# Kernel tuning notes

Measured on AMD Instinct MI355X. Metric: run time of the kernel, lower is better.

The kernel has to match this reference:

```python
import jax, jax.numpy as jnp
import numpy as np

# Attention(d_model=1024, d_head=64, h=16, fastmax=True) -> fastmax_custom path with
# mask=True, normalize=True, temperature=1, a0=1, a1=1, lim=1, p=1, zero RPE.
B, N, D_MODEL, H, D_HEAD = 1, 2048, 1024, 16, 64
A0, A1, LIM = 1.0, 1.0, 1.0


def setup_inputs() -> dict:
    key = jax.random.key(0)
    ks = jax.random.split(key, 6)
    s = 1.0 / np.sqrt(D_MODEL).astype(np.float32)
    return {
        "X": jax.random.normal(ks[0], (B, N, D_MODEL), jnp.float32),
        "Wq": jax.random.normal(ks[1], (H * D_HEAD, D_MODEL), jnp.float32) * s,
        "Wk": jax.random.normal(ks[2], (H * D_HEAD, D_MODEL), jnp.float32) * s,
        "Wv": jax.random.normal(ks[3], (H * D_HEAD, D_MODEL), jnp.float32) * s,
        "Wo": jax.random.normal(ks[4], (D_MODEL, H * D_HEAD), jnp.float32) * s,
        "bo": jnp.zeros((D_MODEL,), jnp.float32),
    }


def _fastmax_causal_p1(q, k, v):
    # q,k,v: [b,h,n,d]. fastmax normalize: scale q,k so the max per-token L2 norm
    # (over the sequence, per batch-head) equals LIM; temperature forced to 1.
    qn = jnp.max(jnp.linalg.norm(q, axis=-1), axis=-1)[..., None, None]  # [b,h,1,1]
    kn = jnp.max(jnp.linalg.norm(k, axis=-1), axis=-1)[..., None, None]
    q = LIM * q / qn
    k = LIM * k / kn
    n = q.shape[2]
    # first-order (p=1) polynomial kernel attention, causal via prefix sums:
    #   score(i,j) = a0 + a1 * <q_i, k_j>,  j <= i
    kv = jnp.cumsum(k[..., :, None] * v[..., None, :], axis=2)  # [b,h,n,d,d]
    num = A0 * jnp.cumsum(v, axis=2) + A1 * jnp.einsum('bhnd,bhnde->bhne', q, kv)
    ksum = jnp.cumsum(k, axis=2)  # [b,h,n,d]
    den = A0 * jnp.arange(1, n + 1, dtype=q.dtype) + A1 * jnp.einsum('bhnd,bhnd->bhn', q, ksum)
    return num / den[..., None]


def reference(X, Wq, Wk, Wv, Wo, bo):
    b, n, _ = X.shape

    def heads(W):
        # [b,n,d_model] @ [d_model,h*d] -> [b,h,n,d]
        return (X @ W.T).reshape(b, n, H, D_HEAD).transpose(0, 2, 1, 3)

    q, k, v = heads(Wq), heads(Wk), heads(Wv)
    vh = _fastmax_causal_p1(q, k, v)                       # [b,h,n,d]
    vh = vh.transpose(0, 2, 1, 3).reshape(b, n, H * D_HEAD)
    return vh @ Wo.T + bo                                  # eval mode: dropout is identity
```

## Files before the change

### kernel.cpp

```cpp
#include <hip/hip_runtime.h>

#define N_SEQ 2048
#define NH 16
#define DH 64
#define CHUNK 64
#define NCHUNK 32

typedef float f32x4 __attribute__((ext_vector_type(4)));
typedef __bf16 bf16x8 __attribute__((ext_vector_type(8)));
typedef unsigned short u16x4 __attribute__((ext_vector_type(4)));
typedef unsigned short u16x8 __attribute__((ext_vector_type(8)));

static __device__ inline unsigned short f2b(float x) {
    unsigned int u = __builtin_bit_cast(unsigned int, x);
    unsigned int r = (u + 0x7fffu + ((u >> 16) & 1u)) >> 16;
    return (unsigned short)r;
}
static __device__ inline float b2f(unsigned short b) {
    return __builtin_bit_cast(float, (unsigned int)b << 16);
}
static __device__ inline int sw(int row, int col) {
    return row * 64 + (col ^ ((row & 7) << 3));
}

__global__ __launch_bounds__(256) void cast_all(
    const float* __restrict__ X, const float* __restrict__ Wq, const float* __restrict__ Wk,
    const float* __restrict__ Wv, const float* __restrict__ Wo,
    unsigned short* __restrict__ Xb, unsigned short* __restrict__ Wb,
    unsigned short* __restrict__ Wob, float* __restrict__ nrm) {
    if (blockIdx.x == 0 && threadIdx.x < 32) nrm[threadIdx.x] = 0.f;
    int i = blockIdx.x * 256 + threadIdx.x;
    const float* src; unsigned short* dst; int off;
    if (i < 524288)       { src = X;  dst = Xb;               off = i; }
    else if (i < 786432)  { src = Wq; dst = Wb;               off = i - 524288; }
    else if (i < 1048576) { src = Wk; dst = Wb + (1u << 20);  off = i - 786432; }
    else if (i < 1310720) { src = Wv; dst = Wb + (2u << 20);  off = i - 1048576; }
    else                  { src = Wo; dst = Wob;              off = i - 1310720; }
    float4 v = reinterpret_cast<const float4*>(src)[off];
    u16x4 o;
    o[0] = f2b(v.x); o[1] = f2b(v.y); o[2] = f2b(v.z); o[3] = f2b(v.w);
    reinterpret_cast<u16x4*>(dst)[off] = o;
}

static __device__ inline void gload_lds16(const unsigned short* g, unsigned short* l) {
    __builtin_amdgcn_global_load_lds(
        (const __attribute__((address_space(1))) unsigned int*)g,
        (__attribute__((address_space(3))) unsigned int*)l, 16, 0, 0);
}

template<int MODE, int BM>
__global__ __launch_bounds__(256, 2) void gemm_bf16(
    const unsigned short* __restrict__ A,
    const unsigned short* __restrict__ B,
    float* __restrict__ outf,
    unsigned short* __restrict__ outb,
    const float* __restrict__ bias,
    float* __restrict__ nrm,
    int M, int N, int K)
{
    __shared__ __align__(16) unsigned short As[BM][64];
    __shared__ __align__(16) unsigned short Bs[128][64];

    const int L = blockIdx.y * gridDim.x + blockIdx.x;
    const int cpx = (gridDim.x * gridDim.y) >> 3;
    const int tile = (L & 7) * cpx + (L >> 3);
    const int bn = tile / gridDim.y;
    const int bm = tile % gridDim.y;

    const int t = threadIdx.x;
    const int wave = t >> 6, lane = t & 63;
    const int wm = wave >> 1, wn = wave & 1;
    const int r16 = lane & 15, ks = lane >> 4;
    constexpr int MFRAG = BM / 32;

    f32x4 acc[MFRAG][4] = {};

    const unsigned short* gA = A + (size_t)bm * BM * K;
    const unsigned short* gB = B + (size_t)bn * 128 * K;
    const int lrow = lane >> 3;
    const int scol = (((lane & 7) ^ (lrow & 7)) << 3);
    const int rsw = (r16 & 7) << 3;

    for (int k0 = 0; k0 < K; k0 += 64) {
        __syncthreads();
        #pragma unroll
        for (int g = 0; g < BM / 32; ++g) {
            int r0 = wave * (BM / 4) + g * 8;
            gload_lds16(&gA[(size_t)(r0 + lrow) * K + k0 + scol], &As[r0][0]);
        }
        #pragma unroll
        for (int g = 0; g < 4; ++g) {
            int r0 = wave * 32 + g * 8;
            gload_lds16(&gB[(size_t)(r0 + lrow) * K + k0 + scol], &Bs[r0][0]);
        }
        __syncthreads();

        #pragma unroll
        for (int ksub = 0; ksub < 2; ++ksub) {
            const int sl = (((ksub << 2) + ks) << 3) ^ rsw;
            bf16x8 af[MFRAG], bfr[4];
            #pragma unroll
            for (int m = 0; m < MFRAG; ++m)
                af[m] = *reinterpret_cast<const bf16x8*>(&As[wm * (BM / 2) + m * 16 + r16][sl]);
            #pragma unroll
            for (int n = 0; n < 4; ++n)
                bfr[n] = *reinterpret_cast<const bf16x8*>(&Bs[wn * 64 + n * 16 + r16][sl]);
            #pragma unroll
            for (int m = 0; m < MFRAG; ++m)
                #pragma unroll
                for (int n = 0; n < 4; ++n)
                    acc[m][n] = __builtin_amdgcn_mfma_f32_16x16x32_bf16(af[m], bfr[n], acc[m][n], 0, 0, 0);
        }
    }

    #pragma unroll
    for (int m = 0; m < MFRAG; ++m) {
        int row0 = bm * BM + wm * (BM / 2) + m * 16 + ks * 4;
        #pragma unroll
        for (int n = 0; n < 4; ++n) {
            int col = bn * 128 + wn * 64 + n * 16 + r16;
            if (MODE == 0) {
                int wch = col >> 10, h = (col >> 6) & 15, d = col & 63;
                unsigned short* dst = outb + (size_t)wch * (NH * (size_t)N_SEQ * DH)
                                          + (size_t)h * N_SEQ * DH + d;
                #pragma unroll
                for (int j = 0; j < 4; ++j)
                    dst[(size_t)(row0 + j) * DH] = f2b(acc[m][n][j]);
            } else {
                float bv = bias[col];
                #pragma unroll
                for (int j = 0; j < 4; ++j)
                    outf[(size_t)(row0 + j) * N + col] = acc[m][n][j] + bv;
            }
        }
    }

    if (MODE == 0) {
        const int colbase = bn * 128 + wn * 64;
        const int wch = colbase >> 10;
        if (wch < 2) {
            const int h = (colbase >> 6) & 15;
            float mx = 0.f;
            #pragma unroll
            for (int m = 0; m < MFRAG; ++m)
                #pragma unroll
                for (int j = 0; j < 4; ++j) {
                    float rs = 0.f;
                    #pragma unroll
                    for (int n = 0; n < 4; ++n) rs = fmaf(acc[m][n][j], acc[m][n][j], rs);
                    rs += __shfl_xor(rs, 1);
                    rs += __shfl_xor(rs, 2);
                    rs += __shfl_xor(rs, 4);
                    rs += __shfl_xor(rs, 8);
                    mx = fmaxf(mx, rs);
                }
            mx = fmaxf(mx, __shfl_xor(mx, 16));
            mx = fmaxf(mx, __shfl_xor(mx, 32));
            if (lane == 0)
                atomicMax(reinterpret_cast<unsigned int*>(&nrm[wch * 16 + h]),
                          __builtin_bit_cast(unsigned int, mx));
        }
    }
}

__global__ __launch_bounds__(256) void chunk_sums(const unsigned short* __restrict__ Kb,
                                                  const unsigned short* __restrict__ Vb,
                                                  unsigned short* __restrict__ Ssum,
                                                  float* __restrict__ zsum,
                                                  float* __restrict__ vssum) {
    const int h = blockIdx.x >> 5, c = blockIdx.x & 31;
    __shared__ __align__(16) unsigned short Kt[4096];
    __shared__ __align__(16) unsigned short Vt[4096];
    const size_t off = ((size_t)h * N_SEQ + c * CHUNK) * DH;
    const int t = threadIdx.x, lane = t & 63;

    {
        const int d = t & 63, j0 = (t >> 6) * 16;
        unsigned short rk[16], rv[16];
        #pragma unroll
        for (int i = 0; i < 16; ++i) {
            rk[i] = Kb[off + (size_t)(j0 + i) * DH + d];
            rv[i] = Vb[off + (size_t)(j0 + i) * DH + d];
        }
        u16x8 a, b;
        #pragma unroll
        for (int i = 0; i < 8; ++i) { a[i] = rk[i]; b[i] = rk[8 + i]; }
        *reinterpret_cast<u16x8*>(&Kt[sw(d, j0)]) = a;
        *reinterpret_cast<u16x8*>(&Kt[sw(d, j0 + 8)]) = b;
        #pragma unroll
        for (int i = 0; i < 8; ++i) { a[i] = rv[i]; b[i] = rv[8 + i]; }
        *reinterpret_cast<u16x8*>(&Vt[sw(d, j0)]) = a;
        *reinterpret_cast<u16x8*>(&Vt[sw(d, j0 + 8)]) = b;
    }
    __syncthreads();

    const int w = t >> 6, cl = lane & 15, g = lane >> 4;
    bf16x8 ak0 = *reinterpret_cast<const bf16x8*>(&Kt[sw(w * 16 + cl, g * 8)]);
    bf16x8 ak1 = *reinterpret_cast<const bf16x8*>(&Kt[sw(w * 16 + cl, 32 + g * 8)]);
    f32x4 acc[4] = {};
    #pragma unroll
    for (int et = 0; et < 4; ++et) {
        bf16x8 b0 = *reinterpret_cast<const bf16x8*>(&Vt[sw(et * 16 + cl, g * 8)]);
        bf16x8 b1 = *reinterpret_cast<const bf16x8*>(&Vt[sw(et * 16 + cl, 32 + g * 8)]);
        acc[et] = __builtin_amdgcn_mfma_f32_16x16x32_bf16(ak0, b0, acc[et], 0, 0, 0);
        acc[et] = __builtin_amdgcn_mfma_f32_16x16x32_bf16(ak1, b1, acc[et], 0, 0, 0);
    }
    unsigned short* So = Ssum + (size_t)blockIdx.x * (DH * DH);
    #pragma unroll
    for (int et = 0; et < 4; ++et)
        #pragma unroll
        for (int j = 0; j < 4; ++j)
            So[(size_t)(w * 16 + g * 4 + j) * DH + et * 16 + cl] = f2b(acc[et][j]);

    if (t < 64) {
        float z = 0.f;
        #pragma unroll
        for (int i = 0; i < 8; ++i) {
            u16x8 v = *reinterpret_cast<const u16x8*>(&Kt[sw(t, i * 8)]);
            #pragma unroll
            for (int k = 0; k < 8; ++k) z += b2f(v[k]);
        }
        zsum[(size_t)blockIdx.x * DH + t] = z;
    } else if (t < 128) {
        int e = t - 64;
        float z = 0.f;
        #pragma unroll
        for (int i = 0; i < 8; ++i) {
            u16x8 v = *reinterpret_cast<const u16x8*>(&Vt[sw(e, i * 8)]);
            #pragma unroll
            for (int k = 0; k < 8; ++k) z += b2f(v[k]);
        }
        vssum[(size_t)blockIdx.x * DH + e] = z;
    }
}

__global__ __launch_bounds__(256) void chunk_scan(unsigned short* __restrict__ Ssum,
                                                  float* __restrict__ zsum,
                                                  float* __restrict__ vssum) {
    const int b = blockIdx.x;
    if (b < 256) {
        const int h = b >> 4;
        const int e = (b & 15) * 256 + threadIdx.x;
        size_t base = (size_t)h * NCHUNK * (DH * DH) + e;
        float run = 0.f;
        for (int c = 0; c < NCHUNK; ++c) {
            size_t idx = base + (size_t)c * (DH * DH);
            float tmp = b2f(Ssum[idx]); Ssum[idx] = f2b(run); run += tmp;
        }
    } else {
        const int g = (b - 256) * 256 + threadIdx.x;
        const int which = g >> 10, h = (g >> 6) & 15, e = g & 63;
        float* arr = which ? vssum : zsum;
        size_t base = (size_t)h * NCHUNK * DH + e;
        float run = 0.f;
        for (int c = 0; c < NCHUNK; ++c) {
            size_t idx = base + (size_t)c * DH;
            float tmp = arr[idx]; arr[idx] = run; run += tmp;
        }
    }
}

__global__ __launch_bounds__(256) void intra_attn(
    const unsigned short* __restrict__ Qb, const unsigned short* __restrict__ Kb,
    const unsigned short* __restrict__ Vb,
    const unsigned short* __restrict__ Ssum, const float* __restrict__ zsum,
    const float* __restrict__ vssum, const float* __restrict__ nrm,
    unsigned short* __restrict__ vhb) {
    const int h = blockIdx.x >> 5, c = blockIdx.x & 31;
    __shared__ __align__(16) unsigned short Ql[4096];
    __shared__ __align__(16) unsigned short Kl[4096];
    __shared__ __align__(16) unsigned short Vt[4096];
    __shared__ __align__(16) unsigned short Sp[4096];
    __shared__ __align__(16) unsigned short Pl[4096];
    __shared__ float zp[DH], vsp[DH];

    const int t = threadIdx.x, lane = t & 63, w = t >> 6;
    const float alpha = 1.f / sqrtf(nrm[h] * nrm[16 + h]);
    const size_t off = ((size_t)h * N_SEQ + c * CHUNK) * DH;

    #pragma unroll
    for (int p = 0; p < 2; ++p) {
        int lin = t + p * 256;
        int row = lin >> 3, col = (lin & 7) * 8;
        u16x8 q = *reinterpret_cast<const u16x8*>(Qb + off + (size_t)row * DH + col);
        u16x8 k = *reinterpret_cast<const u16x8*>(Kb + off + (size_t)row * DH + col);
        *reinterpret_cast<u16x8*>(&Ql[sw(row, col)]) = q;
        *reinterpret_cast<u16x8*>(&Kl[sw(row, col)]) = k;
    }
    {
        const int e = t & 63, j0 = (t >> 6) * 16;
        unsigned short rv[16];
        #pragma unroll
        for (int i = 0; i < 16; ++i) rv[i] = Vb[off + (size_t)(j0 + i) * DH + e];
        u16x8 a, b;
        #pragma unroll
        for (int i = 0; i < 8; ++i) { a[i] = rv[i]; b[i] = rv[8 + i]; }
        *reinterpret_cast<u16x8*>(&Vt[sw(e, j0)]) = a;
        *reinterpret_cast<u16x8*>(&Vt[sw(e, j0 + 8)]) = b;
    }
    {
        const unsigned short* Sg = Ssum + (size_t)blockIdx.x * (DH * DH);
        const int e = t & 63, d0 = (t >> 6) * 16;
        u16x8 a, b;
        #pragma unroll
        for (int i = 0; i < 8; ++i) a[i] = f2b(alpha * b2f(Sg[(size_t)(d0 + i) * DH + e]));
        #pragma unroll
        for (int i = 0; i < 8; ++i) b[i] = f2b(alpha * b2f(Sg[(size_t)(d0 + 8 + i) * DH + e]));
        *reinterpret_cast<u16x8*>(&Sp[sw(e, d0)]) = a;
        *reinterpret_cast<u16x8*>(&Sp[sw(e, d0 + 8)]) = b;
    }
    if (t < 64) zp[t] = alpha * zsum[(size_t)blockIdx.x * DH + t];
    else if (t < 128) vsp[t - 64] = vssum[(size_t)blockIdx.x * DH + (t - 64)];
    __syncthreads();

    const int cl = lane & 15, g = lane >> 4;
    const int qrow = (w << 4) + cl;

    bf16x8 aq0 = *reinterpret_cast<const bf16x8*>(&Ql[sw(qrow, g * 8)]);
    bf16x8 aq1 = *reinterpret_cast<const bf16x8*>(&Ql[sw(qrow, 32 + g * 8)]);

    f32x4 acc[4] = {};
    #pragma unroll
    for (int et = 0; et < 4; ++et) {
        bf16x8 b0 = *reinterpret_cast<const bf16x8*>(&Sp[sw(et * 16 + cl, g * 8)]);
        bf16x8 b1 = *reinterpret_cast<const bf16x8*>(&Sp[sw(et * 16 + cl, 32 + g * 8)]);
        acc[et] = __builtin_amdgcn_mfma_f32_16x16x32_bf16(aq0, b0, acc[et], 0, 0, 0);
        acc[et] = __builtin_amdgcn_mfma_f32_16x16x32_bf16(aq1, b1, acc[et], 0, 0, 0);
    }
    f32x4 sacc[4] = {};
    #pragma unroll
    for (int kt = 0; kt < 4; ++kt) {
        bf16x8 b0 = *reinterpret_cast<const bf16x8*>(&Kl[sw(kt * 16 + cl, g * 8)]);
        bf16x8 b1 = *reinterpret_cast<const bf16x8*>(&Kl[sw(kt * 16 + cl, 32 + g * 8)]);
        sacc[kt] = __builtin_amdgcn_mfma_f32_16x16x32_bf16(aq0, b0, sacc[kt], 0, 0, 0);
        sacc[kt] = __builtin_amdgcn_mfma_f32_16x16x32_bf16(aq1, b1, sacc[kt], 0, 0, 0);
    }
    unsigned short* Pw = &Pl[w * 1024];
    float part[4] = {0.f, 0.f, 0.f, 0.f};
    #pragma unroll
    for (int kt = 0; kt < 4; ++kt) {
        int key = kt * 16 + cl;
        #pragma unroll
        for (int j = 0; j < 4; ++j) {
            int rr = g * 4 + j;
            int q = (w << 4) + rr;
            float s = (key <= q) ? fmaf(alpha, sacc[kt][j], 1.f) : 0.f;
            part[j] += s;
            Pw[rr * 64 + (key ^ ((rr & 7) << 3))] = f2b(s);
        }
    }
    #pragma unroll
    for (int j = 0; j < 4; ++j) {
        int q = (w << 4) + g * 4 + j;
        float qz = 0.f;
        #pragma unroll
        for (int m = 0; m < 4; ++m) {
            int d = cl + m * 16;
            qz = fmaf(b2f(Ql[sw(q, d)]), zp[d], qz);
        }
        part[j] += qz;
    }
    #pragma unroll
    for (int o = 1; o < 16; o <<= 1)
        #pragma unroll
        for (int j = 0; j < 4; ++j) part[j] += __shfl_xor(part[j], o);
    float invden[4];
    #pragma unroll
    for (int j = 0; j < 4; ++j) invden[j] = 1.f / ((float)(c * CHUNK) + part[j]);

    #pragma unroll
    for (int ks = 0; ks < 2; ++ks) {
        bf16x8 ap = *reinterpret_cast<const bf16x8*>(&Pw[cl * 64 + ((ks * 32 + g * 8) ^ ((cl & 7) << 3))]);
        #pragma unroll
        for (int et = 0; et < 4; ++et) {
            bf16x8 bv = *reinterpret_cast<const bf16x8*>(&Vt[sw(et * 16 + cl, ks * 32 + g * 8)]);
            acc[et] = __builtin_amdgcn_mfma_f32_16x16x32_bf16(ap, bv, acc[et], 0, 0, 0);
        }
    }
    #pragma unroll
    for (int et = 0; et < 4; ++et)
        #pragma unroll
        for (int j = 0; j < 4; ++j) {
            int q = (w << 4) + g * 4 + j;
            int e = et * 16 + cl;
            float o = (vsp[e] + acc[et][j]) * invden[j];
            vhb[(size_t)(c * CHUNK + q) * (NH * DH) + h * DH + e] = f2b(o);
        }
}

extern "C" void kernel_launch(void* const* d_in, const int* in_sizes, int n_in,
                              void* d_out, int out_size, void* d_ws, size_t ws_size,
                              hipStream_t stream) {
    const float* X  = (const float*)d_in[0];
    const float* Wq = (const float*)d_in[1];
    const float* Wk = (const float*)d_in[2];
    const float* Wv = (const float*)d_in[3];
    const float* Wo = (const float*)d_in[4];
    const float* bo = (const float*)d_in[5];
    float* out = (float*)d_out;

    char* w = (char*)d_ws;
    unsigned short* Xb   = (unsigned short*)(w);
    unsigned short* Wb   = (unsigned short*)(w + (4u  << 20));
    unsigned short* Wob  = (unsigned short*)(w + (10u << 20));
    unsigned short* Qb   = (unsigned short*)(w + (12u << 20));
    unsigned short* vhb  = (unsigned short*)(w + (24u << 20));
    float*          nrm  = (float*)(w + (28u << 20));
    unsigned short* Ssum = (unsigned short*)(w + (29u << 20));
    float*          zsum = (float*)(w + (34u << 20));
    float*          vssum= (float*)(w + (34u << 20) + (1u << 17));
    unsigned short* Kb = Qb + 2097152;
    unsigned short* Vb = Qb + 2u * 2097152;

    cast_all<<<6144, 256, 0, stream>>>(X, Wq, Wk, Wv, Wo, Xb, Wb, Wob, nrm);
    gemm_bf16<0, 128><<<dim3(24, 16), 256, 0, stream>>>(Xb, Wb, nullptr, Qb, nullptr, nrm, 2048, 3072, 1024);
    chunk_sums<<<512, 256, 0, stream>>>(Kb, Vb, Ssum, zsum, vssum);
    chunk_scan<<<264, 256, 0, stream>>>(Ssum, zsum, vssum);
    intra_attn<<<512, 256, 0, stream>>>(Qb, Kb, Vb, Ssum, zsum, vssum, nrm, vhb);
    gemm_bf16<1, 64><<<dim3(8, 32), 256, 0, stream>>>(vhb, Wob, out, nullptr, bo, nullptr, 2048, 1024, 1024);
}
```

Baseline: 68.50 us.

## Double-buffer GEMM LDS tiles and fuse chunk-sum, scan, attention into cooperative kernel

The GEMM now uses two LDS stages and issues the next K-tile's async global-to-LDS loads before computing the current tile, so load latency overlaps MFMA work. The three mid kernels (chunk sums, prefix scan, intra-chunk attention) are merged into one cooperative kernel separated by grid-wide syncs, which removes two launches and reuses the V tile already in LDS. This requires all 512 blocks to be co-resident (2 per CU). Grid syncs add their own overhead, and the doubled LDS in the GEMM may reduce occupancy.

```diff
diff --git a/kernel.cpp b/kernel.cpp
--- a/kernel.cpp
+++ b/kernel.cpp
@@ -1,4 +1,7 @@
 #include <hip/hip_runtime.h>
+#include <hip/hip_cooperative_groups.h>
+
+namespace cg = cooperative_groups;
 
 #define N_SEQ 2048
 #define NH 16
@@ -58,8 +61,8 @@
     float* __restrict__ nrm,
     int M, int N, int K)
 {
-    __shared__ __align__(16) unsigned short As[BM][64];
-    __shared__ __align__(16) unsigned short Bs[128][64];
+    __shared__ __align__(16) unsigned short As[2][BM][64];
+    __shared__ __align__(16) unsigned short Bs[2][128][64];
 
     const int L = blockIdx.y * gridDim.x + blockIdx.x;
     const int cpx = (gridDim.x * gridDim.y) >> 3;
@@ -80,37 +83,45 @@
     const int lrow = lane >> 3;
     const int scol = (((lane & 7) ^ (lrow & 7)) << 3);
     const int rsw = (r16 & 7) << 3;
-
-    for (int k0 = 0; k0 < K; k0 += 64) {
-        __syncthreads();
-        #pragma unroll
-        for (int g = 0; g < BM / 32; ++g) {
-            int r0 = wave * (BM / 4) + g * 8;
-            gload_lds16(&gA[(size_t)(r0 + lrow) * K + k0 + scol], &As[r0][0]);
-        }
-        #pragma unroll
-        for (int g = 0; g < 4; ++g) {
-            int r0 = wave * 32 + g * 8;
-            gload_lds16(&gB[(size_t)(r0 + lrow) * K + k0 + scol], &Bs[r0][0]);
-        }
-        __syncthreads();
-
+    const int NIT = K >> 6;
+
+    auto stage = [&](int it, int pp) {
+        const int k0 = it << 6;
+        #pragma unroll
+        for (int g2 = 0; g2 < BM / 32; ++g2) {
+            int r0 = wave * (BM / 4) + g2 * 8;
+            gload_lds16(&gA[(size_t)(r0 + lrow) * K + k0 + scol], &As[pp][r0][0]);
+        }
+        #pragma unroll
+        for (int g2 = 0; g2 < 4; ++g2) {
+            int r0 = wave * 32 + g2 * 8;
+            gload_lds16(&gB[(size_t)(r0 + lrow) * K + k0 + scol], &Bs[pp][r0][0]);
+        }
+    };
+
+    stage(0, 0);
+    __syncthreads();
+    int pp = 0;
+    for (int it = 0; it < NIT; ++it) {
+        if (it + 1 < NIT) stage(it + 1, pp ^ 1);
         #pragma unroll
         for (int ksub = 0; ksub < 2; ++ksub) {
             const int sl = (((ksub << 2) + ks) << 3) ^ rsw;
             bf16x8 af[MFRAG], bfr[4];
             #pragma unroll
             for (int m = 0; m < MFRAG; ++m)
-                af[m] = *reinterpret_cast<const bf16x8*>(&As[wm * (BM / 2) + m * 16 + r16][sl]);
+                af[m] = *reinterpret_cast<const bf16x8*>(&As[pp][wm * (BM / 2) + m * 16 + r16][sl]);
             #pragma unroll
             for (int n = 0; n < 4; ++n)
-                bfr[n] = *reinterpret_cast<const bf16x8*>(&Bs[wn * 64 + n * 16 + r16][sl]);
+                bfr[n] = *reinterpret_cast<const bf16x8*>(&Bs[pp][wn * 64 + n * 16 + r16][sl]);
             #pragma unroll
             for (int m = 0; m < MFRAG; ++m)
                 #pragma unroll
                 for (int n = 0; n < 4; ++n)
                     acc[m][n] = __builtin_amdgcn_mfma_f32_16x16x32_bf16(af[m], bfr[n], acc[m][n], 0, 0, 0);
         }
+        pp ^= 1;
+        if (it + 1 < NIT) __syncthreads();
     }
 
     #pragma unroll
@@ -163,16 +174,25 @@
     }
 }
 
-__global__ __launch_bounds__(256) void chunk_sums(const unsigned short* __restrict__ Kb,
-                                                  const unsigned short* __restrict__ Vb,
-                                                  unsigned short* __restrict__ Ssum,
-                                                  float* __restrict__ zsum,
-                                                  float* __restrict__ vssum) {
-    const int h = blockIdx.x >> 5, c = blockIdx.x & 31;
-    __shared__ __align__(16) unsigned short Kt[4096];
-    __shared__ __align__(16) unsigned short Vt[4096];
+__global__ __launch_bounds__(256, 2) void mid_kernel(
+    const unsigned short* __restrict__ Qb, const unsigned short* __restrict__ Kb,
+    const unsigned short* __restrict__ Vb,
+    unsigned short* __restrict__ Ssum, float* __restrict__ zsum, float* __restrict__ vssum,
+    const float* __restrict__ nrm, unsigned short* __restrict__ vhb)
+{
+    __shared__ __align__(16) unsigned short sm[5 * 4096];
+    __shared__ float zpvs[2 * DH];
+    unsigned short* s0 = sm;
+    unsigned short* s1 = sm + 4096;
+    unsigned short* s2 = sm + 2 * 4096;
+    unsigned short* s3 = sm + 3 * 4096;
+    unsigned short* s4 = sm + 4 * 4096;
+
+    const int b = blockIdx.x;
+    const int h = b >> 5, c = b & 31;
+    const int t = threadIdx.x, lane = t & 63, w = t >> 6;
     const size_t off = ((size_t)h * N_SEQ + c * CHUNK) * DH;
-    const int t = threadIdx.x, lane = t & 63;
+    const int cl = lane & 15, g = lane >> 4;
 
     {
         const int d = t & 63, j0 = (t >> 6) * 16;
@@ -182,160 +202,126 @@
             rk[i] = Kb[off + (size_t)(j0 + i) * DH + d];
             rv[i] = Vb[off + (size_t)(j0 + i) * DH + d];
         }
-        u16x8 a, b;
-        #pragma unroll
-        for (int i = 0; i < 8; ++i) { a[i] = rk[i]; b[i] = rk[8 + i]; }
-        *reinterpret_cast<u16x8*>(&Kt[sw(d, j0)]) = a;
-        *reinterpret_cast<u16x8*>(&Kt[sw(d, j0 + 8)]) = b;
-        #pragma unroll
-        for (int i = 0; i < 8; ++i) { a[i] = rv[i]; b[i] = rv[8 + i]; }
-        *reinterpret_cast<u16x8*>(&Vt[sw(d, j0)]) = a;
-        *reinterpret_cast<u16x8*>(&Vt[sw(d, j0 + 8)]) = b;
+        u16x8 a2, b2;
+        #pragma unroll
+        for (int i = 0; i < 8; ++i) { a2[i] = rk[i]; b2[i] = rk[8 + i]; }
+        *reinterpret_cast<u16x8*>(&s0[sw(d, j0)]) = a2;
+        *reinterpret_cast<u16x8*>(&s0[sw(d, j0 + 8)]) = b2;
+        #pragma unroll
+        for (int i = 0; i < 8; ++i) { a2[i] = rv[i]; b2[i] = rv[8 + i]; }
+        *reinterpret_cast<u16x8*>(&s2[sw(d, j0)]) = a2;
+        *reinterpret_cast<u16x8*>(&s2[sw(d, j0 + 8)]) = b2;
     }
     __syncthreads();
-
-    const int w = t >> 6, cl = lane & 15, g = lane >> 4;
-    bf16x8 ak0 = *reinterpret_cast<const bf16x8*>(&Kt[sw(w * 16 + cl, g * 8)]);
-    bf16x8 ak1 = *reinterpret_cast<const bf16x8*>(&Kt[sw(w * 16 + cl, 32 + g * 8)]);
-    f32x4 acc[4] = {};
-    #pragma unroll
-    for (int et = 0; et < 4; ++et) {
-        bf16x8 b0 = *reinterpret_cast<const bf16x8*>(&Vt[sw(et * 16 + cl, g * 8)]);
-        bf16x8 b1 = *reinterpret_cast<const bf16x8*>(&Vt[sw(et * 16 + cl, 32 + g * 8)]);
-        acc[et] = __builtin_amdgcn_mfma_f32_16x16x32_bf16(ak0, b0, acc[et], 0, 0, 0);
-        acc[et] = __builtin_amdgcn_mfma_f32_16x16x32_bf16(ak1, b1, acc[et], 0, 0, 0);
-    }
-    unsigned short* So = Ssum + (size_t)blockIdx.x * (DH * DH);
-    #pragma unroll
-    for (int et = 0; et < 4; ++et)
-        #pragma unroll
-        for (int j = 0; j < 4; ++j)
-            So[(size_t)(w * 16 + g * 4 + j) * DH + et * 16 + cl] = f2b(acc[et][j]);
-
-    if (t < 64) {
-        float z = 0.f;
-        #pragma unroll
-        for (int i = 0; i < 8; ++i) {
-            u16x8 v = *reinterpret_cast<const u16x8*>(&Kt[sw(t, i * 8)]);
-            #pragma unroll
-            for (int k = 0; k < 8; ++k) z += b2f(v[k]);
-        }
-        zsum[(size_t)blockIdx.x * DH + t] = z;
-    } else if (t < 128) {
-        int e = t - 64;
-        float z = 0.f;
-        #pragma unroll
-        for (int i = 0; i < 8; ++i) {
-            u16x8 v = *reinterpret_cast<const u16x8*>(&Vt[sw(e, i * 8)]);
-            #pragma unroll
-            for (int k = 0; k < 8; ++k) z += b2f(v[k]);
-        }
-        vssum[(size_t)blockIdx.x * DH + e] = z;
-    }
-}
-
-__global__ __launch_bounds__(256) void chunk_scan(unsigned short* __restrict__ Ssum,
-                                                  float* __restrict__ zsum,
-                                                  float* __restrict__ vssum) {
-    const int b = blockIdx.x;
+    {
+        bf16x8 ak0 = *reinterpret_cast<const bf16x8*>(&s0[sw(w * 16 + cl, g * 8)]);
+        bf16x8 ak1 = *reinterpret_cast<const bf16x8*>(&s0[sw(w * 16 + cl, 32 + g * 8)]);
+        f32x4 acc[4] = {};
+        #pragma unroll
+        for (int et = 0; et < 4; ++et) {
+            bf16x8 b0 = *reinterpret_cast<const bf16x8*>(&s2[sw(et * 16 + cl, g * 8)]);
+            bf16x8 b1 = *reinterpret_cast<const bf16x8*>(&s2[sw(et * 16 + cl, 32 + g * 8)]);
+            acc[et] = __builtin_amdgcn_mfma_f32_16x16x32_bf16(ak0, b0, acc[et], 0, 0, 0);
+            acc[et] = __builtin_amdgcn_mfma_f32_16x16x32_bf16(ak1, b1, acc[et], 0, 0, 0);
+        }
+        unsigned short* So = Ssum + (size_t)b * (DH * DH);
+        #pragma unroll
+        for (int et = 0; et < 4; ++et)
+            #pragma unroll
+            for (int j = 0; j < 4; ++j)
+                So[(size_t)(w * 16 + g * 4 + j) * DH + et * 16 + cl] = f2b(acc[et][j]);
+
+        if (t < 64) {
+            float z = 0.f;
+            #pragma unroll
+            for (int i = 0; i < 8; ++i) {
+                u16x8 v = *reinterpret_cast<const u16x8*>(&s0[sw(t, i * 8)]);
+                #pragma unroll
+                for (int k2 = 0; k2 < 8; ++k2) z += b2f(v[k2]);
+            }
+            zsum[(size_t)b * DH + t] = z;
+        } else if (t < 128) {
+            int e = t - 64;
+            float z = 0.f;
+            #pragma unroll
+            for (int i = 0; i < 8; ++i) {
+                u16x8 v = *reinterpret_cast<const u16x8*>(&s2[sw(e, i * 8)]);
+                #pragma unroll
+                for (int k2 = 0; k2 < 8; ++k2) z += b2f(v[k2]);
+            }
+            vssum[(size_t)b * DH + e] = z;
+        }
+    }
+    cg::this_grid().sync();
+
     if (b < 256) {
-        const int h = b >> 4;
-        const int e = (b & 15) * 256 + threadIdx.x;
-        size_t base = (size_t)h * NCHUNK * (DH * DH) + e;
+        const int hh = b >> 4;
+        const int e = (b & 15) * 256 + t;
+        size_t base = (size_t)hh * NCHUNK * (DH * DH) + e;
         float run = 0.f;
-        for (int c = 0; c < NCHUNK; ++c) {
-            size_t idx = base + (size_t)c * (DH * DH);
+        for (int cc = 0; cc < NCHUNK; ++cc) {
+            size_t idx = base + (size_t)cc * (DH * DH);
             float tmp = b2f(Ssum[idx]); Ssum[idx] = f2b(run); run += tmp;
         }
-    } else {
-        const int g = (b - 256) * 256 + threadIdx.x;
-        const int which = g >> 10, h = (g >> 6) & 15, e = g & 63;
+    } else if (b < 264) {
+        const int g2 = (b - 256) * 256 + t;
+        const int which = g2 >> 10, hh = (g2 >> 6) & 15, e = g2 & 63;
         float* arr = which ? vssum : zsum;
-        size_t base = (size_t)h * NCHUNK * DH + e;
+        size_t base = (size_t)hh * NCHUNK * DH + e;
         float run = 0.f;
-        for (int c = 0; c < NCHUNK; ++c) {
-            size_t idx = base + (size_t)c * DH;
+        for (int cc = 0; cc < NCHUNK; ++cc) {
+            size_t idx = base + (size_t)cc * DH;
             float tmp = arr[idx]; arr[idx] = run; run += tmp;
         }
     }
-}
-
-__global__ __launch_bounds__(256) void intra_attn(
-    const unsigned short* __restrict__ Qb, const unsigned short* __restrict__ Kb,
-    const unsigned short* __restrict__ Vb,
-    const unsigned short* __restrict__ Ssum, const float* __restrict__ zsum,
-    const float* __restrict__ vssum, const float* __restrict__ nrm,
-    unsigned short* __restrict__ vhb) {
-    const int h = blockIdx.x >> 5, c = blockIdx.x & 31;
-    __shared__ __align__(16) unsigned short Ql[4096];
-    __shared__ __align__(16) unsigned short Kl[4096];
-    __shared__ __align__(16) unsigned short Vt[4096];
-    __shared__ __align__(16) unsigned short Sp[4096];
-    __shared__ __align__(16) unsigned short Pl[4096];
-    __shared__ float zp[DH], vsp[DH];
-
-    const int t = threadIdx.x, lane = t & 63, w = t >> 6;
+    cg::this_grid().sync();
+
     const float alpha = 1.f / sqrtf(nrm[h] * nrm[16 + h]);
-    const size_t off = ((size_t)h * N_SEQ + c * CHUNK) * DH;
-
     #pragma unroll
     for (int p = 0; p < 2; ++p) {
         int lin = t + p * 256;
         int row = lin >> 3, col = (lin & 7) * 8;
         u16x8 q = *reinterpret_cast<const u16x8*>(Qb + off + (size_t)row * DH + col);
         u16x8 k = *reinterpret_cast<const u16x8*>(Kb + off + (size_t)row * DH + col);
-        *reinterpret_cast<u16x8*>(&Ql[sw(row, col)]) = q;
-        *reinterpret_cast<u16x8*>(&Kl[sw(row, col)]) = k;
+        *reinterpret_cast<u16x8*>(&s0[sw(row, col)]) = q;
+        *reinterpret_cast<u16x8*>(&s1[sw(row, col)]) = k;
     }
     {
-        const int e = t & 63, j0 = (t >> 6) * 16;
-        unsigned short rv[16];
-        #pragma unroll
-        for (int i = 0; i < 16; ++i) rv[i] = Vb[off + (size_t)(j0 + i) * DH + e];
-        u16x8 a, b;
-        #pragma unroll
-        for (int i = 0; i < 8; ++i) { a[i] = rv[i]; b[i] = rv[8 + i]; }
-        *reinterpret_cast<u16x8*>(&Vt[sw(e, j0)]) = a;
-        *reinterpret_cast<u16x8*>(&Vt[sw(e, j0 + 8)]) = b;
-    }
-    {
-        const unsigned short* Sg = Ssum + (size_t)blockIdx.x * (DH * DH);
+        const unsigned short* Sg = Ssum + (size_t)b * (DH * DH);
         const int e = t & 63, d0 = (t >> 6) * 16;
-        u16x8 a, b;
-        #pragma unroll
-        for (int i = 0; i < 8; ++i) a[i] = f2b(alpha * b2f(Sg[(size_t)(d0 + i) * DH + e]));
-        #pragma unroll
-        for (int i = 0; i < 8; ++i) b[i] = f2b(alpha * b2f(Sg[(size_t)(d0 + 8 + i) * DH + e]));
-        *reinterpret_cast<u16x8*>(&Sp[sw(e, d0)]) = a;
-        *reinterpret_cast<u16x8*>(&Sp[sw(e, d0 + 8)]) = b;
-    }
-    if (t < 64) zp[t] = alpha * zsum[(size_t)blockIdx.x * DH + t];
-    else if (t < 128) vsp[t - 64] = vssum[(size_t)blockIdx.x * DH + (t - 64)];
+        u16x8 a2, b2;
+        #pragma unroll
+        for (int i = 0; i < 8; ++i) a2[i] = f2b(alpha * b2f(Sg[(size_t)(d0 + i) * DH + e]));
+        #pragma unroll
+        for (int i = 0; i < 8; ++i) b2[i] = f2b(alpha * b2f(Sg[(size_t)(d0 + 8 + i) * DH + e]));
+        *reinterpret_cast<u16x8*>(&s3[sw(e, d0)]) = a2;
+        *reinterpret_cast<u16x8*>(&s3[sw(e, d0 + 8)]) = b2;
+    }
+    if (t < 64) zpvs[t] = alpha * zsum[(size_t)b * DH + t];
+    else if (t < 128) zpvs[t] = vssum[(size_t)b * DH + (t - 64)];
     __syncthreads();
 
-    const int cl = lane & 15, g = lane >> 4;
     const int qrow = (w << 4) + cl;
-
-    bf16x8 aq0 = *reinterpret_cast<const bf16x8*>(&Ql[sw(qrow, g * 8)]);
-    bf16x8 aq1 = *reinterpret_cast<const bf16x8*>(&Ql[sw(qrow, 32 + g * 8)]);
+    bf16x8 aq0 = *reinterpret_cast<const bf16x8*>(&s0[sw(qrow, g * 8)]);
+    bf16x8 aq1 = *reinterpret_cast<const bf16x8*>(&s0[sw(qrow, 32 + g * 8)]);
 
     f32x4 acc[4] = {};
     #pragma unroll
     for (int et = 0; et < 4; ++et) {
-        bf16x8 b0 = *reinterpret_cast<const bf16x8*>(&Sp[sw(et * 16 + cl, g * 8)]);
-        bf16x8 b1 = *reinterpret_cast<const bf16x8*>(&Sp[sw(et * 16 + cl, 32 + g * 8)]);
+        bf16x8 b0 = *reinterpret_cast<const bf16x8*>(&s3[sw(et * 16 + cl, g * 8)]);
+        bf16x8 b1 = *reinterpret_cast<const bf16x8*>(&s3[sw(et * 16 + cl, 32 + g * 8)]);
         acc[et] = __builtin_amdgcn_mfma_f32_16x16x32_bf16(aq0, b0, acc[et], 0, 0, 0);
         acc[et] = __builtin_amdgcn_mfma_f32_16x16x32_bf16(aq1, b1, acc[et], 0, 0, 0);
     }
     f32x4 sacc[4] = {};
     #pragma unroll
     for (int kt = 0; kt < 4; ++kt) {
-        bf16x8 b0 = *reinterpret_cast<const bf16x8*>(&Kl[sw(kt * 16 + cl, g * 8)]);
-        bf16x8 b1 = *reinterpret_cast<const bf16x8*>(&Kl[sw(kt * 16 + cl, 32 + g * 8)]);
+        bf16x8 b0 = *reinterpret_cast<const bf16x8*>(&s1[sw(kt * 16 + cl, g * 8)]);
+        bf16x8 b1 = *reinterpret_cast<const bf16x8*>(&s1[sw(kt * 16 + cl, 32 + g * 8)]);
         sacc[kt] = __builtin_amdgcn_mfma_f32_16x16x32_bf16(aq0, b0, sacc[kt], 0, 0, 0);
         sacc[kt] = __builtin_amdgcn_mfma_f32_16x16x32_bf16(aq1, b1, sacc[kt], 0, 0, 0);
     }
-    unsigned short* Pw = &Pl[w * 1024];
+    unsigned short* Pw = &s4[w * 1024];
     float part[4] = {0.f, 0.f, 0.f, 0.f};
     #pragma unroll
     for (int kt = 0; kt < 4; ++kt) {
@@ -356,7 +342,7 @@
         #pragma unroll
         for (int m = 0; m < 4; ++m) {
             int d = cl + m * 16;
-            qz = fmaf(b2f(Ql[sw(q, d)]), zp[d], qz);
+            qz = fmaf(b2f(s0[sw(q, d)]), zpvs[d], qz);
         }
         part[j] += qz;
     }
@@ -369,11 +355,11 @@
     for (int j = 0; j < 4; ++j) invden[j] = 1.f / ((float)(c * CHUNK) + part[j]);
 
     #pragma unroll
-    for (int ks = 0; ks < 2; ++ks) {
-        bf16x8 ap = *reinterpret_cast<const bf16x8*>(&Pw[cl * 64 + ((ks * 32 + g * 8) ^ ((cl & 7) << 3))]);
+    for (int ks2 = 0; ks2 < 2; ++ks2) {
+        bf16x8 ap = *reinterpret_cast<const bf16x8*>(&Pw[cl * 64 + ((ks2 * 32 + g * 8) ^ ((cl & 7) << 3))]);
         #pragma unroll
         for (int et = 0; et < 4; ++et) {
-            bf16x8 bv = *reinterpret_cast<const bf16x8*>(&Vt[sw(et * 16 + cl, ks * 32 + g * 8)]);
+            bf16x8 bv = *reinterpret_cast<const bf16x8*>(&s2[sw(et * 16 + cl, ks2 * 32 + g * 8)]);
             acc[et] = __builtin_amdgcn_mfma_f32_16x16x32_bf16(ap, bv, acc[et], 0, 0, 0);
         }
     }
@@ -383,7 +369,7 @@
         for (int j = 0; j < 4; ++j) {
             int q = (w << 4) + g * 4 + j;
             int e = et * 16 + cl;
-            float o = (vsp[e] + acc[et][j]) * invden[j];
+            float o = (zpvs[64 + e] + acc[et][j]) * invden[j];
             vhb[(size_t)(c * CHUNK + q) * (NH * DH) + h * DH + e] = f2b(o);
         }
 }
@@ -414,8 +400,10 @@
 
     cast_all<<<6144, 256, 0, stream>>>(X, Wq, Wk, Wv, Wo, Xb, Wb, Wob, nrm);
     gemm_bf16<0, 128><<<dim3(24, 16), 256, 0, stream>>>(Xb, Wb, nullptr, Qb, nullptr, nrm, 2048, 3072, 1024);
-    chunk_sums<<<512, 256, 0, stream>>>(Kb, Vb, Ssum, zsum, vssum);
-    chunk_scan<<<264, 256, 0, stream>>>(Ssum, zsum, vssum);
-    intra_attn<<<512, 256, 0, stream>>>(Qb, Kb, Vb, Ssum, zsum, vssum, nrm, vhb);
+    {
+        void* args[] = { (void*)&Qb, (void*)&Kb, (void*)&Vb, (void*)&Ssum,
+                         (void*)&zsum, (void*)&vssum, (void*)&nrm, (void*)&vhb };
+        hipLaunchCooperativeKernel((const void*)mid_kernel, dim3(512), dim3(256), args, 0, stream);
+    }
     gemm_bf16<1, 64><<<dim3(8, 32), 256, 0, stream>>>(vhb, Wob, out, nullptr, bo, nullptr, 2048, 1024, 1024);
 }
```

Result: slower. 204.3 us (+198.2%).

## Double-buffer LDS tiles in bf16 GEMM to overlap global loads with MFMA

Applied to the files above, without the earlier changes.

The GEMM kernel gets two LDS buffers for the A and B tiles. The next K-tile is now prefetched with global_load_lds while MFMAs run on the current tile, and one barrier per iteration replaces the previous two. This targets the load-latency stall at each K step. It doubles LDS use per block, which may lower occupancy under the 2-blocks-per-SM launch bound. Correctness depends on the barrier also waiting for the outstanding direct-to-LDS loads.

```diff
diff --git a/kernel.cpp b/kernel.cpp
--- a/kernel.cpp
+++ b/kernel.cpp
@@ -58,8 +58,8 @@
     float* __restrict__ nrm,
     int M, int N, int K)
 {
-    __shared__ __align__(16) unsigned short As[BM][64];
-    __shared__ __align__(16) unsigned short Bs[128][64];
+    __shared__ __align__(16) unsigned short As[2][BM][64];
+    __shared__ __align__(16) unsigned short Bs[2][128][64];
 
     const int L = blockIdx.y * gridDim.x + blockIdx.x;
     const int cpx = (gridDim.x * gridDim.y) >> 3;
@@ -80,37 +80,45 @@
     const int lrow = lane >> 3;
     const int scol = (((lane & 7) ^ (lrow & 7)) << 3);
     const int rsw = (r16 & 7) << 3;
-
-    for (int k0 = 0; k0 < K; k0 += 64) {
-        __syncthreads();
-        #pragma unroll
-        for (int g = 0; g < BM / 32; ++g) {
-            int r0 = wave * (BM / 4) + g * 8;
-            gload_lds16(&gA[(size_t)(r0 + lrow) * K + k0 + scol], &As[r0][0]);
-        }
-        #pragma unroll
-        for (int g = 0; g < 4; ++g) {
-            int r0 = wave * 32 + g * 8;
-            gload_lds16(&gB[(size_t)(r0 + lrow) * K + k0 + scol], &Bs[r0][0]);
-        }
-        __syncthreads();
-
+    const int NIT = K >> 6;
+
+    auto stage = [&](int it, int pp) {
+        const int k0 = it << 6;
+        #pragma unroll
+        for (int g2 = 0; g2 < BM / 32; ++g2) {
+            int r0 = wave * (BM / 4) + g2 * 8;
+            gload_lds16(&gA[(size_t)(r0 + lrow) * K + k0 + scol], &As[pp][r0][0]);
+        }
+        #pragma unroll
+        for (int g2 = 0; g2 < 4; ++g2) {
+            int r0 = wave * 32 + g2 * 8;
+            gload_lds16(&gB[(size_t)(r0 + lrow) * K + k0 + scol], &Bs[pp][r0][0]);
+        }
+    };
+
+    stage(0, 0);
+    __syncthreads();
+    int pp = 0;
+    for (int it = 0; it < NIT; ++it) {
+        if (it + 1 < NIT) stage(it + 1, pp ^ 1);
         #pragma unroll
         for (int ksub = 0; ksub < 2; ++ksub) {
             const int sl = (((ksub << 2) + ks) << 3) ^ rsw;
             bf16x8 af[MFRAG], bfr[4];
             #pragma unroll
             for (int m = 0; m < MFRAG; ++m)
-                af[m] = *reinterpret_cast<const bf16x8*>(&As[wm * (BM / 2) + m * 16 + r16][sl]);
+                af[m] = *reinterpret_cast<const bf16x8*>(&As[pp][wm * (BM / 2) + m * 16 + r16][sl]);
             #pragma unroll
             for (int n = 0; n < 4; ++n)
-                bfr[n] = *reinterpret_cast<const bf16x8*>(&Bs[wn * 64 + n * 16 + r16][sl]);
+                bfr[n] = *reinterpret_cast<const bf16x8*>(&Bs[pp][wn * 64 + n * 16 + r16][sl]);
             #pragma unroll
             for (int m = 0; m < MFRAG; ++m)
                 #pragma unroll
                 for (int n = 0; n < 4; ++n)
                     acc[m][n] = __builtin_amdgcn_mfma_f32_16x16x32_bf16(af[m], bfr[n], acc[m][n], 0, 0, 0);
         }
+        pp ^= 1;
+        if (it + 1 < NIT) __syncthreads();
     }
 
     #pragma unroll
```

After: 69.08 us. About the same (+0.8%).

## Split QKV GEMM into dedicated kernel using 32x32 MFMA and per-head tiles

Applied to the files above, without the earlier changes.

The templated GEMM is split into a QKV projection kernel and an output projection kernel. The QKV kernel now uses 128x64 tiles (one head per column tile, 768 blocks) with 32x32x16 bf16 MFMA instructions. The per-token norm reduction moves to a shared-memory combine across the two column waves before the atomicMax. The aim is more blocks for better CU occupancy and fewer LDS fragment loads per MFMA, at the cost of halving B-tile reuse and adding a block barrier in the norm epilogue.

```diff
diff --git a/kernel.cpp b/kernel.cpp
--- a/kernel.cpp
+++ b/kernel.cpp
@@ -7,6 +7,7 @@
 #define NCHUNK 32
 
 typedef float f32x4 __attribute__((ext_vector_type(4)));
+typedef float f32x16 __attribute__((ext_vector_type(16)));
 typedef __bf16 bf16x8 __attribute__((ext_vector_type(8)));
 typedef unsigned short u16x4 __attribute__((ext_vector_type(4)));
 typedef unsigned short u16x8 __attribute__((ext_vector_type(8)));
@@ -48,18 +49,16 @@
         (__attribute__((address_space(3))) unsigned int*)l, 16, 0, 0);
 }
 
-template<int MODE, int BM>
-__global__ __launch_bounds__(256, 2) void gemm_bf16(
+__global__ __launch_bounds__(256, 2) void gemm_qkv(
     const unsigned short* __restrict__ A,
     const unsigned short* __restrict__ B,
-    float* __restrict__ outf,
     unsigned short* __restrict__ outb,
-    const float* __restrict__ bias,
     float* __restrict__ nrm,
-    int M, int N, int K)
+    int K)
 {
-    __shared__ __align__(16) unsigned short As[BM][64];
-    __shared__ __align__(16) unsigned short Bs[128][64];
+    __shared__ __align__(16) unsigned short As[128][64];
+    __shared__ __align__(16) unsigned short Bs[64][64];
+    __shared__ float pnorm[2][128];
 
     const int L = blockIdx.y * gridDim.x + blockIdx.x;
     const int cpx = (gridDim.x * gridDim.y) >> 3;
@@ -70,12 +69,106 @@
     const int t = threadIdx.x;
     const int wave = t >> 6, lane = t & 63;
     const int wm = wave >> 1, wn = wave & 1;
+    const int l31 = lane & 31, lhi = lane >> 5;
+
+    f32x16 acc0 = {};
+    f32x16 acc1 = {};
+
+    const unsigned short* gA = A + (size_t)bm * 128 * K;
+    const unsigned short* gB = B + (size_t)bn * 64 * K;
+    const int lrow = lane >> 3;
+    const int scol = (((lane & 7) ^ (lrow & 7)) << 3);
+
+    for (int k0 = 0; k0 < K; k0 += 64) {
+        __syncthreads();
+        #pragma unroll
+        for (int g2 = 0; g2 < 4; ++g2) {
+            int r0 = wave * 32 + g2 * 8;
+            gload_lds16(&gA[(size_t)(r0 + lrow) * K + k0 + scol], &As[r0][0]);
+        }
+        #pragma unroll
+        for (int g2 = 0; g2 < 2; ++g2) {
+            int r0 = wave * 16 + g2 * 8;
+            gload_lds16(&gB[(size_t)(r0 + lrow) * K + k0 + scol], &Bs[r0][0]);
+        }
+        __syncthreads();
+
+        #pragma unroll
+        for (int ks2 = 0; ks2 < 4; ++ks2) {
+            const int cb = (ks2 * 16 + (lhi << 3)) ^ ((lane & 7) << 3);
+            bf16x8 a0 = *reinterpret_cast<const bf16x8*>(&As[wm * 64 + l31][cb]);
+            bf16x8 a1 = *reinterpret_cast<const bf16x8*>(&As[wm * 64 + 32 + l31][cb]);
+            bf16x8 bb = *reinterpret_cast<const bf16x8*>(&Bs[wn * 32 + l31][cb]);
+            acc0 = __builtin_amdgcn_mfma_f32_32x32x16_bf16(a0, bb, acc0, 0, 0, 0);
+            acc1 = __builtin_amdgcn_mfma_f32_32x32x16_bf16(a1, bb, acc1, 0, 0, 0);
+        }
+    }
+
+    const int wch = bn >> 4;
+    const int h = bn & 15;
+    const int d = wn * 32 + l31;
+    unsigned short* dst = outb + (size_t)wch * (NH * (size_t)N_SEQ * DH)
+                               + (size_t)h * N_SEQ * DH + d;
+    #pragma unroll
+    for (int r = 0; r < 16; ++r) {
+        int crow = (r & 3) + 8 * (r >> 2) + 4 * lhi;
+        int row0 = bm * 128 + wm * 64 + crow;
+        dst[(size_t)row0 * DH] = f2b(acc0[r]);
+        dst[(size_t)(row0 + 32) * DH] = f2b(acc1[r]);
+    }
+
+    if (wch < 2) {
+        #pragma unroll
+        for (int r = 0; r < 16; ++r) {
+            int crow = (r & 3) + 8 * (r >> 2) + 4 * lhi;
+            float r0 = acc0[r] * acc0[r];
+            float r1 = acc1[r] * acc1[r];
+            #pragma unroll
+            for (int o = 1; o < 32; o <<= 1) {
+                r0 += __shfl_xor(r0, o);
+                r1 += __shfl_xor(r1, o);
+            }
+            if (l31 == 0) {
+                pnorm[wn][wm * 64 + crow] = r0;
+                pnorm[wn][wm * 64 + 32 + crow] = r1;
+            }
+        }
+        __syncthreads();
+        if (t < 128) {
+            float s = pnorm[0][t] + pnorm[1][t];
+            #pragma unroll
+            for (int o = 1; o < 64; o <<= 1) s = fmaxf(s, __shfl_xor(s, o));
+            if ((t & 63) == 0)
+                atomicMax(reinterpret_cast<unsigned int*>(&nrm[wch * 16 + h]),
+                          __builtin_bit_cast(unsigned int, s));
+        }
+    }
+}
+
+__global__ __launch_bounds__(256, 2) void gemm_out(
+    const unsigned short* __restrict__ A,
+    const unsigned short* __restrict__ B,
+    float* __restrict__ outf,
+    const float* __restrict__ bias,
+    int N, int K)
+{
+    __shared__ __align__(16) unsigned short As[64][64];
+    __shared__ __align__(16) unsigned short Bs[128][64];
+
+    const int L = blockIdx.y * gridDim.x + blockIdx.x;
+    const int cpx = (gridDim.x * gridDim.y) >> 3;
+    const int tile = (L & 7) * cpx + (L >> 3);
+    const int bn = tile / gridDim.y;
+    const int bm = tile % gridDim.y;
+
+    const int t = threadIdx.x;
+    const int wave = t >> 6, lane = t & 63;
+    const int wm = wave >> 1, wn = wave & 1;
     const int r16 = lane & 15, ks = lane >> 4;
-    constexpr int MFRAG = BM / 32;
-
-    f32x4 acc[MFRAG][4] = {};
-
-    const unsigned short* gA = A + (size_t)bm * BM * K;
+
+    f32x4 acc[2][4] = {};
+
+    const unsigned short* gA = A + (size_t)bm * 64 * K;
     const unsigned short* gB = B + (size_t)bn * 128 * K;
     const int lrow = lane >> 3;
     const int scol = (((lane & 7) ^ (lrow & 7)) << 3);
@@ -84,13 +177,13 @@
     for (int k0 = 0; k0 < K; k0 += 64) {
         __syncthreads();
         #pragma unroll
-        for (int g = 0; g < BM / 32; ++g) {
-            int r0 = wave * (BM / 4) + g * 8;
+        for (int g2 = 0; g2 < 2; ++g2) {
+            int r0 = wave * 16 + g2 * 8;
             gload_lds16(&gA[(size_t)(r0 + lrow) * K + k0 + scol], &As[r0][0]);
         }
         #pragma unroll
-        for (int g = 0; g < 4; ++g) {
-            int r0 = wave * 32 + g * 8;
+        for (int g2 = 0; g2 < 4; ++g2) {
+            int r0 = wave * 32 + g2 * 8;
             gload_lds16(&gB[(size_t)(r0 + lrow) * K + k0 + scol], &Bs[r0][0]);
         }
         __syncthreads();
@@ -98,15 +191,15 @@
         #pragma unroll
         for (int ksub = 0; ksub < 2; ++ksub) {
             const int sl = (((ksub << 2) + ks) << 3) ^ rsw;
-            bf16x8 af[MFRAG], bfr[4];
-            #pragma unroll
-            for (int m = 0; m < MFRAG; ++m)
-                af[m] = *reinterpret_cast<const bf16x8*>(&As[wm * (BM / 2) + m * 16 + r16][sl]);
+            bf16x8 af[2], bfr[4];
+            #pragma unroll
+            for (int m = 0; m < 2; ++m)
+                af[m] = *reinterpret_cast<const bf16x8*>(&As[wm * 32 + m * 16 + r16][sl]);
             #pragma unroll
             for (int n = 0; n < 4; ++n)
                 bfr[n] = *reinterpret_cast<const bf16x8*>(&Bs[wn * 64 + n * 16 + r16][sl]);
             #pragma unroll
-            for (int m = 0; m < MFRAG; ++m)
+            for (int m = 0; m < 2; ++m)
                 #pragma unroll
                 for (int n = 0; n < 4; ++n)
                     acc[m][n] = __builtin_amdgcn_mfma_f32_16x16x32_bf16(af[m], bfr[n], acc[m][n], 0, 0, 0);
@@ -114,51 +207,15 @@
     }
 
     #pragma unroll
-    for (int m = 0; m < MFRAG; ++m) {
-        int row0 = bm * BM + wm * (BM / 2) + m * 16 + ks * 4;
+    for (int m = 0; m < 2; ++m) {
+        int row0 = bm * 64 + wm * 32 + m * 16 + ks * 4;
         #pragma unroll
         for (int n = 0; n < 4; ++n) {
             int col = bn * 128 + wn * 64 + n * 16 + r16;
-            if (MODE == 0) {
-                int wch = col >> 10, h = (col >> 6) & 15, d = col & 63;
-                unsigned short* dst = outb + (size_t)wch * (NH * (size_t)N_SEQ * DH)
-                                          + (size_t)h * N_SEQ * DH + d;
-                #pragma unroll
-                for (int j = 0; j < 4; ++j)
-                    dst[(size_t)(row0 + j) * DH] = f2b(acc[m][n][j]);
-            } else {
-                float bv = bias[col];
-                #pragma unroll
-                for (int j = 0; j < 4; ++j)
-                    outf[(size_t)(row0 + j) * N + col] = acc[m][n][j] + bv;
-            }
-        }
-    }
-
-    if (MODE == 0) {
-        const int colbase = bn * 128 + wn * 64;
-        const int wch = colbase >> 10;
-        if (wch < 2) {
-            const int h = (colbase >> 6) & 15;
-            float mx = 0.f;
-            #pragma unroll
-            for (int m = 0; m < MFRAG; ++m)
-                #pragma unroll
-                for (int j = 0; j < 4; ++j) {
-                    float rs = 0.f;
-                    #pragma unroll
-                    for (int n = 0; n < 4; ++n) rs = fmaf(acc[m][n][j], acc[m][n][j], rs);
-                    rs += __shfl_xor(rs, 1);
-                    rs += __shfl_xor(rs, 2);
-                    rs += __shfl_xor(rs, 4);
-                    rs += __shfl_xor(rs, 8);
-                    mx = fmaxf(mx, rs);
-                }
-            mx = fmaxf(mx, __shfl_xor(mx, 16));
-            mx = fmaxf(mx, __shfl_xor(mx, 32));
-            if (lane == 0)
-                atomicMax(reinterpret_cast<unsigned int*>(&nrm[wch * 16 + h]),
-                          __builtin_bit_cast(unsigned int, mx));
+            float bv = bias[col];
+            #pragma unroll
+            for (int j = 0; j < 4; ++j)
+                outf[(size_t)(row0 + j) * N + col] = acc[m][n][j] + bv;
         }
     }
 }
@@ -413,9 +470,9 @@
     unsigned short* Vb = Qb + 2u * 2097152;
 
     cast_all<<<6144, 256, 0, stream>>>(X, Wq, Wk, Wv, Wo, Xb, Wb, Wob, nrm);
-    gemm_bf16<0, 128><<<dim3(24, 16), 256, 0, stream>>>(Xb, Wb, nullptr, Qb, nullptr, nrm, 2048, 3072, 1024);
+    gemm_qkv<<<dim3(48, 16), 256, 0, stream>>>(Xb, Wb, Qb, nrm, 1024);
     chunk_sums<<<512, 256, 0, stream>>>(Kb, Vb, Ssum, zsum, vssum);
     chunk_scan<<<264, 256, 0, stream>>>(Ssum, zsum, vssum);
     intra_attn<<<512, 256, 0, stream>>>(Qb, Kb, Vb, Ssum, zsum, vssum, nrm, vhb);
-    gemm_bf16<1, 64><<<dim3(8, 32), 256, 0, stream>>>(vhb, Wob, out, nullptr, bo, nullptr, 2048, 1024, 1024);
-}
+    gemm_out<<<dim3(8, 32), 256, 0, stream>>>(vhb, Wob, out, bo, 1024, 1024);
+}
```

After: 69.00 us. No clear change (+0.7%).
